# Kernel tuning notes

Measured on AMD Instinct MI355X. Metric: run time of the kernel, lower is better.

Reference implementation:

```python
import jax, jax.numpy as jnp
import numpy as np

E = 576        # embed_dims
HEADS = 18
NPTS = 12
NF = 3         # num_frames
DD = 2 * NF - 1  # depth of value volume (5)
HD = E // HEADS  # head dim (32)


def _grid_init_bias():
    # Faithful reproduction of init_weights() for sampling_offsets.bias
    theta = np.arange(8) * (2.0 * np.pi / 8)
    yaw = np.stack([np.cos(theta), np.sin(theta), np.zeros(8)], -1)
    roll = np.stack([np.zeros(8), np.cos(theta), np.sin(theta)], -1)
    pitch = np.stack([np.cos(theta), np.zeros(8), np.sin(theta)], -1)
    g = np.concatenate([yaw, pitch[[1, 2, 3, 5, 6, 7]], roll[[1, 3, 5, 7]]], 0)  # (18,3)
    g = g / np.abs(g).max(-1, keepdims=True)
    g = np.tile(g[:, None, None, :], (1, 1, NPTS, 1))              # (18,1,12,3)
    g = g * np.arange(1, NPTS + 1, dtype=np.float64)[None, None, :, None]
    return g.reshape(-1).astype(np.float32)                        # (18*12*3,)


def setup_inputs() -> dict:
    key = jax.random.key(0)
    ks = jax.random.split(key, 6)
    bs, h, w = 2, 64, 80
    nq = h * w
    lim = float(np.sqrt(6.0 / (E + E)))  # xavier uniform for square E x E
    return {
        "query": jax.random.normal(ks[0], (bs, nq, E), jnp.float32),
        "value": jax.random.normal(ks[1], (bs, nq * DD, E), jnp.float32),
        "query_pos": jax.random.normal(ks[2], (bs, nq, E), jnp.float32),
        "W_off": jnp.zeros((E, HEADS * NPTS * 3), jnp.float32),  # constant_init 0
        "b_off": jnp.asarray(_grid_init_bias()),
        "W_attn": jnp.zeros((E, HEADS * NPTS), jnp.float32),
        "b_attn": jnp.zeros((HEADS * NPTS,), jnp.float32),
        "W_v": jax.random.uniform(ks[3], (E, E), jnp.float32, -lim, lim),
        "b_v": jnp.zeros((E,), jnp.float32),
        "W_out": jax.random.uniform(ks[4], (E, E), jnp.float32, -lim, lim),
        "b_out": jnp.zeros((E,), jnp.float32),
        "h": 64,
        "w": 80,
    }


def _deform_attn_3d(value, loc, attn, D, H, W):
    # value: (bs, D*H*W, heads, hd)  token order: depth-major (D, H, W)
    # loc:   (bs, nq, heads, np, 3)  normalized (x, y, z) in [0,1]
    # attn:  (bs, nq, heads, np)
    bs, _, heads, hd = value.shape
    nq = loc.shape[1]
    # (bs, heads, D*H*W, hd) flat spatial for gathers
    v = value.reshape(bs, D, H, W, heads, hd).transpose(0, 4, 1, 2, 3, 5)
    v = v.reshape(bs, heads, D * H * W, hd)
    lt = jnp.moveaxis(loc, 2, 1)    # (bs, heads, nq, np, 3)
    at = jnp.moveaxis(attn, 2, 1)   # (bs, heads, nq, np)
    # grid_sample(align_corners=False) coordinate convention: pix = u*size - 0.5
    x = lt[..., 0] * W - 0.5
    y = lt[..., 1] * H - 0.5
    z = lt[..., 2] * D - 0.5
    x0 = jnp.floor(x); y0 = jnp.floor(y); z0 = jnp.floor(z)
    fx = x - x0; fy = y - y0; fz = z - z0
    acc = jnp.zeros((bs, heads, nq, NPTS, hd), v.dtype)
    for dz in (0, 1):
        for dy in (0, 1):
            for dx in (0, 1):
                xi = x0 + dx; yi = y0 + dy; zi = z0 + dz
                wgt = ((fx if dx else 1.0 - fx)
                       * (fy if dy else 1.0 - fy)
                       * (fz if dz else 1.0 - fz))
                valid = ((xi >= 0) & (xi < W) & (yi >= 0) & (yi < H)
                         & (zi >= 0) & (zi < D))
                xc = jnp.clip(xi, 0, W - 1).astype(jnp.int32)
                yc = jnp.clip(yi, 0, H - 1).astype(jnp.int32)
                zc = jnp.clip(zi, 0, D - 1).astype(jnp.int32)
                idx = ((zc * H + yc) * W + xc).reshape(bs, heads, nq * NPTS)
                g = jnp.take_along_axis(v, idx[..., None], axis=2)
                g = g.reshape(bs, heads, nq, NPTS, hd)
                acc = acc + g * (wgt * valid.astype(v.dtype))[..., None]
    out = jnp.einsum("bhqp,bhqpd->bhqd", at, acc)  # softmax-weighted sum over points
    return out.transpose(0, 2, 1, 3).reshape(bs, nq, heads * hd)


def _forward(query, value, query_pos, W_off, b_off, W_attn, b_attn,
             W_v, b_v, W_out, b_out, h, w):
    bs, nq, _ = query.shape
    q = query + query_pos
    v = (value @ W_v + b_v).reshape(bs, nq * DD, HEADS, HD)
    offs = (q @ W_off + b_off).reshape(bs, nq, HEADS, NPTS, 3)
    attn = jax.nn.softmax((q @ W_attn + b_attn).reshape(bs, nq, HEADS, NPTS), axis=-1)
    # reference points: pixel centers normalized, z = 0
    ry, rx = jnp.meshgrid((jnp.arange(h, dtype=jnp.float32) + 0.5) / h,
                          (jnp.arange(w, dtype=jnp.float32) + 0.5) / w,
                          indexing="ij")
    ref = jnp.stack([rx.reshape(-1), ry.reshape(-1),
                     jnp.zeros(h * w, jnp.float32)], -1)  # (nq, 3)
    norm = jnp.array([w, h, NF], jnp.float32)  # NOTE: z normalized by num_frames (as in source)
    loc = ref[None, :, None, None, :] + offs / norm
    out = _deform_attn_3d(v, loc, attn, DD, h, w)
    return out @ W_out + b_out  # dropout is identity at eval


def reference(query, value, query_pos, W_off, b_off, W_attn, b_attn,
              W_v, b_v, W_out, b_out, h, w):
    return _forward(query, value, query_pos, W_off, b_off, W_attn, b_attn,
                    W_v, b_v, W_out, b_out, h, w)
```

## Files before the change

kernel.cpp:

```cpp
#include <hip/hip_runtime.h>
#include <cstdint>

#define E_DIM   576
#define HEADS   18
#define NPTS    12
#define DDEPTH  5
#define HDIM    32
#define BSZ     2
#define GH      64
#define GW      80
#define NQ      (GH*GW)
#define NTOK    (NQ*DDEPTH)
#define MIXW    864
#define BQ_TOT  (BSZ*NQ)

typedef __attribute__((ext_vector_type(8))) short short8;
typedef __attribute__((ext_vector_type(4))) float f32x4;

__device__ __forceinline__ float b2f_lo(uint32_t u) {
    union { uint32_t u; float f; } v; v.u = u << 16; return v.f;
}
__device__ __forceinline__ float b2f_hi(uint32_t u) {
    union { uint32_t u; float f; } v; v.u = u & 0xffff0000u; return v.f;
}
__device__ __forceinline__ ushort f2b(float f) {
    union { float f; uint32_t u; } v; v.f = f;
    return (ushort)((v.u + 0x7fffu + ((v.u >> 16) & 1u)) >> 16);
}

__global__ void prep_all(const float* __restrict__ value,
                         const float* __restrict__ query, const float* __restrict__ query_pos,
                         const float* __restrict__ W_v, const float* __restrict__ W_out,
                         const float* __restrict__ W_off, const float* __restrict__ W_attn,
                         const float* __restrict__ b_off, const float* __restrict__ b_attn,
                         ushort* __restrict__ val_bf16, ushort* __restrict__ q_bf16,
                         ushort* __restrict__ wt_v, ushort* __restrict__ wt_out,
                         ushort* __restrict__ wt_mix, float* __restrict__ bias_mix) {
    const int i = blockIdx.x * blockDim.x + threadIdx.x;
    if (i < 51200 * 576 / 4) {
        const float4 v = reinterpret_cast<const float4*>(value)[i];
        ushort4 o; o.x = f2b(v.x); o.y = f2b(v.y); o.z = f2b(v.z); o.w = f2b(v.w);
        reinterpret_cast<ushort4*>(val_bf16)[i] = o;
    }
    if (i < 10240 * 576 / 4) {
        const float4 va = reinterpret_cast<const float4*>(query)[i];
        const float4 vb = reinterpret_cast<const float4*>(query_pos)[i];
        ushort4 o;
        o.x = f2b(va.x + vb.x); o.y = f2b(va.y + vb.y);
        o.z = f2b(va.z + vb.z); o.w = f2b(va.w + vb.w);
        reinterpret_cast<ushort4*>(q_bf16)[i] = o;
    }
    if (i < 864) bias_mix[i] = (i < 648) ? b_off[i] : b_attn[i - 648];
    if (i < 331776) {
        int n = i / E_DIM, k = i - n * E_DIM;
        wt_v[i] = f2b(W_v[(size_t)k * E_DIM + n]);
    } else if (i < 663552) {
        int j = i - 331776;
        int n = j / E_DIM, k = j - n * E_DIM;
        wt_out[j] = f2b(W_out[(size_t)k * E_DIM + n]);
    } else if (i < 1161216) {
        int j = i - 663552;
        int n = j / E_DIM, k = j - n * E_DIM;
        float v = (n < 648) ? W_off[(size_t)k * 648 + n] : W_attn[(size_t)k * 216 + (n - 648)];
        wt_mix[j] = f2b(v);
    }
}

#define TM 128
#define TN 96
#define BK 32

__device__ __forceinline__ void async_cp16(const ushort* gsrc, ushort* ldst) {
    __builtin_amdgcn_global_load_lds(
        (const __attribute__((address_space(1))) void*)gsrc,
        (__attribute__((address_space(3))) void*)ldst, 16, 0, 0);
}

__device__ __forceinline__ void xcd_map(int id, int total, int nbn, int& bx, int& by) {
    const int xcd = id & 7;
    const int pos = id >> 3;
    const int logical = xcd * (total >> 3) + pos;
    by = logical % nbn;
    bx = logical / nbn;
}

template <typename OutT>
__device__ __forceinline__ void gemm_body(ushort* __restrict__ smem, int bx, int by,
                                          const ushort* __restrict__ A,
                                          const ushort* __restrict__ Bt,
                                          const float* __restrict__ bias,
                                          OutT* __restrict__ C, int K, int ldc) {
    ushort* Asb = smem;
    ushort* Bsb = smem + TM * BK;
    const int tid  = threadIdx.x;
    const int wave = tid >> 6;
    const int lane = tid & 63;
    const int m16  = lane & 15;
    const int quad = lane >> 4;
    const int wr   = wave >> 1;
    const int wc   = wave & 1;
    const int row0 = bx * TM;
    const int n0   = by * TN;

    const f32x4 zero = {0.f, 0.f, 0.f, 0.f};
    f32x4 acc[4][3];
    #pragma unroll
    for (int rt = 0; rt < 4; ++rt)
        #pragma unroll
        for (int ct = 0; ct < 3; ++ct) acc[rt][ct] = zero;

    const int srow = lane >> 2;
    const int scol = (((lane & 3) ^ ((lane >> 3) & 3))) * 8;
    const int ksw  = (quad ^ ((m16 >> 1) & 3)) * 8;

    for (int k0 = 0; k0 < K; k0 += BK) {
        #pragma unroll
        for (int c = 0; c < 2; ++c) {
            const int ch = wave + c * 4;
            async_cp16(A + (size_t)(row0 + ch * 16 + srow) * K + k0 + scol,
                       Asb + ch * 512 + lane * 8);
        }
        async_cp16(Bt + (size_t)(n0 + wave * 16 + srow) * K + k0 + scol,
                   Bsb + wave * 512 + lane * 8);
        if (wave < 2)
            async_cp16(Bt + (size_t)(n0 + (wave + 4) * 16 + srow) * K + k0 + scol,
                       Bsb + (wave + 4) * 512 + lane * 8);
        __syncthreads();

        short8 afrag[4], bfrag[3];
        #pragma unroll
        for (int rt = 0; rt < 4; ++rt)
            afrag[rt] = *reinterpret_cast<const short8*>(
                Asb + (wr * 4 + rt) * 512 + m16 * 32 + ksw);
        #pragma unroll
        for (int ct = 0; ct < 3; ++ct)
            bfrag[ct] = *reinterpret_cast<const short8*>(
                Bsb + (wc * 3 + ct) * 512 + m16 * 32 + ksw);

        #pragma unroll
        for (int rt = 0; rt < 4; ++rt)
            #pragma unroll
            for (int ct = 0; ct < 3; ++ct)
                acc[rt][ct] = __builtin_amdgcn_mfma_f32_16x16x32_bf16(
                    afrag[rt], bfrag[ct], acc[rt][ct], 0, 0, 0);

        __syncthreads();
    }

    #pragma unroll
    for (int ct = 0; ct < 3; ++ct) {
        const int col = n0 + wc * 48 + ct * 16 + m16;
        const float bcol = bias[col];
        #pragma unroll
        for (int rt = 0; rt < 4; ++rt) {
            #pragma unroll
            for (int r = 0; r < 4; ++r) {
                const int row = row0 + wr * 64 + rt * 16 + quad * 4 + r;
                const float val = acc[rt][ct][r] + bcol;
                if constexpr (__is_same(OutT, float)) {
                    C[(size_t)row * ldc + col] = val;
                } else {
                    C[(size_t)row * ldc + col] = f2b(val);
                }
            }
        }
    }
}

template <typename OutT>
__global__ void gemm_mfma(const ushort* __restrict__ A, const ushort* __restrict__ Bt,
                          const float* __restrict__ bias, OutT* __restrict__ C,
                          int K, int ldc, int total, int nbn) {
    __shared__ __align__(16) ushort smem[(TM + TN) * BK];
    int bx, by;
    xcd_map(blockIdx.x, total, nbn, bx, by);
    gemm_body<OutT>(smem, bx, by, A, Bt, bias, C, K, ldc);
}

__global__ void gemm_dual(const ushort* __restrict__ A1, const ushort* __restrict__ B1,
                          const float* __restrict__ bias1, float* __restrict__ C1,
                          int K1, int ldc1, int nbn1, int split,
                          const ushort* __restrict__ A2, const ushort* __restrict__ B2,
                          const float* __restrict__ bias2, ushort* __restrict__ C2,
                          int K2, int ldc2, int nbn2, int total2) {
    __shared__ __align__(16) ushort smem[(TM + TN) * BK];
    const int id = blockIdx.x;
    int bx, by;
    if (id < split) {
        xcd_map(id, split, nbn1, bx, by);
        gemm_body<float>(smem, bx, by, A1, B1, bias1, C1, K1, ldc1);
    } else {
        xcd_map(id - split, total2, nbn2, bx, by);
        gemm_body<ushort>(smem, bx, by, A2, B2, bias2, C2, K2, ldc2);
    }
}

__global__ void __launch_bounds__(256, 8)
deform_kernel(const ushort* __restrict__ vbuf,
              const float* __restrict__ mix,
              ushort* __restrict__ aout) {
    __shared__ uint2 corn[16 * 97];
    __shared__ int   ccnt[16];
    const int gl   = threadIdx.x >> 4;
    const int l    = threadIdx.x & 15;
    const int head = blockIdx.x / 640;
    const int bq   = (blockIdx.x % 640) * 16 + gl;
    const int q    = bq % NQ;
    const int b    = bq / NQ;
    const int qx   = q % GW;
    const int qy   = q / GW;

    const float* mrow = mix + (size_t)bq * MIXW;

    float lg = (l < NPTS) ? mrow[648 + head * NPTS + l] : -1e30f;
    float mx = lg;
    #pragma unroll
    for (int mk = 1; mk < 16; mk <<= 1) mx = fmaxf(mx, __shfl_xor(mx, mk, 16));
    float e = (l < NPTS) ? __expf(lg - mx) : 0.f;
    float s = e;
    #pragma unroll
    for (int mk = 1; mk < 16; mk <<= 1) s += __shfl_xor(s, mk, 16);

    float    cw[8];
    uint32_t coff[8];
    uint32_t mask = 0;
    {
        const float ap = e / s;
        const int pl = (l < NPTS) ? l : 0;
        const int ob = (head * NPTS + pl) * 3;
        const float ox = mrow[ob + 0];
        const float oy = mrow[ob + 1];
        const float oz = mrow[ob + 2];
        const float x = (float)qx + ox;
        const float y = (float)qy + oy;
        const float z = oz * (5.0f / 3.0f) - 0.5f;
        const float x0f = floorf(x), y0f = floorf(y), z0f = floorf(z);
        const int x0 = (int)x0f, y0 = (int)y0f, z0 = (int)z0f;
        const float fx = x - x0f, fy = y - y0f, fz = z - z0f;

        #pragma unroll
        for (int dz = 0; dz < 2; ++dz) {
            const int zi = z0 + dz;
            const bool zv = (zi >= 0) & (zi < DDEPTH);
            const int zc = min(max(zi, 0), DDEPTH - 1);
            const float wz = dz ? fz : 1.f - fz;
            #pragma unroll
            for (int dy = 0; dy < 2; ++dy) {
                const int yi = y0 + dy;
                const bool yv = (yi >= 0) & (yi < GH);
                const int yc = min(max(yi, 0), GH - 1);
                const float wy = dy ? fy : 1.f - fy;
                #pragma unroll
                for (int dx = 0; dx < 2; ++dx) {
                    const int xi = x0 + dx;
                    const bool xv = (xi >= 0) & (xi < GW);
                    const int xc = min(max(xi, 0), GW - 1);
                    const float wx = dx ? fx : 1.f - fx;
                    const int i = dz * 4 + dy * 2 + dx;
                    const bool valid = zv & yv & xv & (l < NPTS);
                    cw[i]   = ap * wz * wy * wx;
                    coff[i] = (uint32_t)((zc * GH + yc) * GW + xc) * (E_DIM / 2);
                    mask |= (valid ? (1u << i) : 0u);
                }
            }
        }
    }

    const int cnt = __popc(mask);
    int pre = cnt;
    #pragma unroll
    for (int mk = 1; mk < 16; mk <<= 1) {
        const int t = __shfl_up(pre, mk, 16);
        if (l >= mk) pre += t;
    }
    int o = gl * 97 + (pre - cnt);
    #pragma unroll
    for (int i = 0; i < 8; ++i) {
        if (mask & (1u << i)) {
            uint2 w; w.x = __float_as_uint(cw[i]); w.y = coff[i];
            corn[o] = w;
            ++o;
        }
    }
    if (l == 15) ccnt[gl] = pre;
    __syncthreads();

    const uint32_t lbase = (uint32_t)b * (uint32_t)(NTOK * (E_DIM / 2))
                         + (uint32_t)(head * (HDIM / 2) + l);
    const uint32_t* vb32 = reinterpret_cast<const uint32_t*>(vbuf);
    const int n = ccnt[gl];
    const uint2* cg = &corn[gl * 97];
    float o0 = 0.f, o1 = 0.f;
    #pragma unroll 2
    for (int j = 0; j < n; ++j) {
        const uint2 wo = cg[j];
        const uint32_t pair = vb32[lbase + wo.y];
        const float w = __uint_as_float(wo.x);
        o0 += w * b2f_lo(pair);
        o1 += w * b2f_hi(pair);
    }
    const uint32_t packed = (uint32_t)f2b(o0) | ((uint32_t)f2b(o1) << 16);
    reinterpret_cast<uint32_t*>(aout)[(size_t)bq * (E_DIM / 2) + head * (HDIM / 2) + l] = packed;
}

extern "C" void kernel_launch(void* const* d_in, const int* in_sizes, int n_in,
                              void* d_out, int out_size, void* d_ws, size_t ws_size,
                              hipStream_t stream) {
    const float* query     = (const float*)d_in[0];
    const float* value     = (const float*)d_in[1];
    const float* query_pos = (const float*)d_in[2];
    const float* W_off     = (const float*)d_in[3];
    const float* b_off     = (const float*)d_in[4];
    const float* W_attn    = (const float*)d_in[5];
    const float* b_attn    = (const float*)d_in[6];
    const float* W_v       = (const float*)d_in[7];
    const float* b_v       = (const float*)d_in[8];
    const float* W_out     = (const float*)d_in[9];
    const float* b_out     = (const float*)d_in[10];
    float* out = (float*)d_out;

    char* ws = (char*)d_ws;
    ushort* vbuf     = (ushort*)(ws);
    ushort* val_bf16 = (ushort*)(ws + 58982400);
    ushort* aout     = val_bf16;
    ushort* q_bf16   = (ushort*)(ws + 117964800);
    float*  mixb     = (float*) (ws + 129761280);
    ushort* wt_v     = (ushort*)(ws + 165150720);
    ushort* wt_out   = (ushort*)(ws + 165814272);
    ushort* wt_mix   = (ushort*)(ws + 166477824);
    float*  bias_mix = (float*) (ws + 167473152);

    prep_all<<<(51200 * 576 / 4) / 256, 256, 0, stream>>>(
        value, query, query_pos, W_v, W_out, W_off, W_attn, b_off, b_attn,
        val_bf16, q_bf16, wt_v, wt_out, wt_mix, bias_mix);

    gemm_dual<<<720 + 2400, 256, 0, stream>>>(
        q_bf16, wt_mix, bias_mix, mixb, E_DIM, MIXW, 9, 720,
        val_bf16, wt_v, b_v, vbuf, E_DIM, E_DIM, 6, 2400);

    deform_kernel<<<HEADS * 640, 256, 0, stream>>>(vbuf, mixb, aout);

    gemm_mfma<float><<<480, 256, 0, stream>>>(
        aout, wt_out, b_out, out, E_DIM, E_DIM, 480, 6);
}
```

Before: 357.5 us.

## Fuse fp32-to-bf16 input conversion and query+pos add into GEMM A-tile loads

Removes the separate prep pass that converted value and query+query_pos to bf16 in global memory. The dual GEMM now loads fp32 A rows directly, adds query_pos for the mix GEMM, converts to bf16 in registers, and writes swizzled tiles into LDS. This avoids a full round-trip of the large value tensor (write and re-read in bf16). The cost is that A loads become synchronous register loads instead of async global-to-LDS copies, and the GEMM reads twice as many bytes for A.

```diff
diff --git a/kernel.cpp b/kernel.cpp
--- a/kernel.cpp
+++ b/kernel.cpp
@@ -16,6 +16,7 @@
 
 typedef __attribute__((ext_vector_type(8))) short short8;
 typedef __attribute__((ext_vector_type(4))) float f32x4;
+typedef __attribute__((ext_vector_type(4))) uint32_t u32x4;
 
 __device__ __forceinline__ float b2f_lo(uint32_t u) {
     union { uint32_t u; float f; } v; v.u = u << 16; return v.f;
@@ -28,38 +29,22 @@
     return (ushort)((v.u + 0x7fffu + ((v.u >> 16) & 1u)) >> 16);
 }
 
-__global__ void prep_all(const float* __restrict__ value,
-                         const float* __restrict__ query, const float* __restrict__ query_pos,
-                         const float* __restrict__ W_v, const float* __restrict__ W_out,
-                         const float* __restrict__ W_off, const float* __restrict__ W_attn,
-                         const float* __restrict__ b_off, const float* __restrict__ b_attn,
-                         ushort* __restrict__ val_bf16, ushort* __restrict__ q_bf16,
-                         ushort* __restrict__ wt_v, ushort* __restrict__ wt_out,
-                         ushort* __restrict__ wt_mix, float* __restrict__ bias_mix) {
-    const int i = blockIdx.x * blockDim.x + threadIdx.x;
-    if (i < 51200 * 576 / 4) {
-        const float4 v = reinterpret_cast<const float4*>(value)[i];
-        ushort4 o; o.x = f2b(v.x); o.y = f2b(v.y); o.z = f2b(v.z); o.w = f2b(v.w);
-        reinterpret_cast<ushort4*>(val_bf16)[i] = o;
-    }
-    if (i < 10240 * 576 / 4) {
-        const float4 va = reinterpret_cast<const float4*>(query)[i];
-        const float4 vb = reinterpret_cast<const float4*>(query_pos)[i];
-        ushort4 o;
-        o.x = f2b(va.x + vb.x); o.y = f2b(va.y + vb.y);
-        o.z = f2b(va.z + vb.z); o.w = f2b(va.w + vb.w);
-        reinterpret_cast<ushort4*>(q_bf16)[i] = o;
-    }
-    if (i < 864) bias_mix[i] = (i < 648) ? b_off[i] : b_attn[i - 648];
-    if (i < 331776) {
-        int n = i / E_DIM, k = i - n * E_DIM;
-        wt_v[i] = f2b(W_v[(size_t)k * E_DIM + n]);
-    } else if (i < 663552) {
-        int j = i - 331776;
+__global__ void prep_weights(const float* __restrict__ W_v, const float* __restrict__ W_out,
+                             const float* __restrict__ W_off, const float* __restrict__ W_attn,
+                             const float* __restrict__ b_off, const float* __restrict__ b_attn,
+                             ushort* __restrict__ wt_v, ushort* __restrict__ wt_out,
+                             ushort* __restrict__ wt_mix, float* __restrict__ bias_mix) {
+    int idx = blockIdx.x * blockDim.x + threadIdx.x;
+    if (idx < 864) bias_mix[idx] = (idx < 648) ? b_off[idx] : b_attn[idx - 648];
+    if (idx < 331776) {
+        int n = idx / E_DIM, k = idx - n * E_DIM;
+        wt_v[idx] = f2b(W_v[(size_t)k * E_DIM + n]);
+    } else if (idx < 663552) {
+        int j = idx - 331776;
         int n = j / E_DIM, k = j - n * E_DIM;
         wt_out[j] = f2b(W_out[(size_t)k * E_DIM + n]);
-    } else if (i < 1161216) {
-        int j = i - 663552;
+    } else if (idx < 1161216) {
+        int j = idx - 663552;
         int n = j / E_DIM, k = j - n * E_DIM;
         float v = (n < 648) ? W_off[(size_t)k * 648 + n] : W_attn[(size_t)k * 216 + (n - 648)];
         wt_mix[j] = f2b(v);
@@ -69,6 +54,10 @@
 #define TM 128
 #define TN 96
 #define BK 32
+
+#define AM_BF16   0
+#define AM_F32    1
+#define AM_F32ADD 2
 
 __device__ __forceinline__ void async_cp16(const ushort* gsrc, ushort* ldst) {
     __builtin_amdgcn_global_load_lds(
@@ -84,9 +73,10 @@
     bx = logical / nbn;
 }
 
-template <typename OutT>
+template <int AMODE, typename OutT>
 __device__ __forceinline__ void gemm_body(ushort* __restrict__ smem, int bx, int by,
-                                          const ushort* __restrict__ A,
+                                          const void* __restrict__ Apv,
+                                          const float* __restrict__ A2,
                                           const ushort* __restrict__ Bt,
                                           const float* __restrict__ bias,
                                           OutT* __restrict__ C, int K, int ldc) {
@@ -113,18 +103,63 @@
     const int scol = (((lane & 3) ^ ((lane >> 3) & 3))) * 8;
     const int ksw  = (quad ^ ((m16 >> 1) & 3)) * 8;
 
+    const int srow_f = ((wave & 1) << 6) | lane;
+    const int khalf  = wave >> 1;
+    const float* A32  = (const float*)Apv;
+    const ushort* A16 = (const ushort*)Apv;
+    const float* arow  = A32 + (size_t)(row0 + srow_f) * K + khalf * 16;
+    const float* arow2 = (AMODE == AM_F32ADD)
+                         ? A2 + (size_t)(row0 + srow_f) * K + khalf * 16 : nullptr;
+
     for (int k0 = 0; k0 < K; k0 += BK) {
-        #pragma unroll
-        for (int c = 0; c < 2; ++c) {
-            const int ch = wave + c * 4;
-            async_cp16(A + (size_t)(row0 + ch * 16 + srow) * K + k0 + scol,
-                       Asb + ch * 512 + lane * 8);
+        float4 av0, av1, av2, av3, bv0, bv1, bv2, bv3;
+        if constexpr (AMODE == AM_BF16) {
+            #pragma unroll
+            for (int c = 0; c < 2; ++c) {
+                const int ch = wave + c * 4;
+                async_cp16(A16 + (size_t)(row0 + ch * 16 + srow) * K + k0 + scol,
+                           Asb + ch * 512 + lane * 8);
+            }
+        } else {
+            av0 = *reinterpret_cast<const float4*>(arow + k0);
+            av1 = *reinterpret_cast<const float4*>(arow + k0 + 4);
+            av2 = *reinterpret_cast<const float4*>(arow + k0 + 8);
+            av3 = *reinterpret_cast<const float4*>(arow + k0 + 12);
+            if constexpr (AMODE == AM_F32ADD) {
+                bv0 = *reinterpret_cast<const float4*>(arow2 + k0);
+                bv1 = *reinterpret_cast<const float4*>(arow2 + k0 + 4);
+                bv2 = *reinterpret_cast<const float4*>(arow2 + k0 + 8);
+                bv3 = *reinterpret_cast<const float4*>(arow2 + k0 + 12);
+            }
         }
         async_cp16(Bt + (size_t)(n0 + wave * 16 + srow) * K + k0 + scol,
                    Bsb + wave * 512 + lane * 8);
         if (wave < 2)
             async_cp16(Bt + (size_t)(n0 + (wave + 4) * 16 + srow) * K + k0 + scol,
                        Bsb + (wave + 4) * 512 + lane * 8);
+
+        if constexpr (AMODE != AM_BF16) {
+            if constexpr (AMODE == AM_F32ADD) {
+                av0.x += bv0.x; av0.y += bv0.y; av0.z += bv0.z; av0.w += bv0.w;
+                av1.x += bv1.x; av1.y += bv1.y; av1.z += bv1.z; av1.w += bv1.w;
+                av2.x += bv2.x; av2.y += bv2.y; av2.z += bv2.z; av2.w += bv2.w;
+                av3.x += bv3.x; av3.y += bv3.y; av3.z += bv3.z; av3.w += bv3.w;
+            }
+            const int r  = srow_f & 15;
+            const int ck = srow_f >> 4;
+            const int xr = (r >> 1) & 3;
+            const int s0 = khalf * 2;
+            u32x4 w0 = {(uint32_t)f2b(av0.x) | ((uint32_t)f2b(av0.y) << 16),
+                        (uint32_t)f2b(av0.z) | ((uint32_t)f2b(av0.w) << 16),
+                        (uint32_t)f2b(av1.x) | ((uint32_t)f2b(av1.y) << 16),
+                        (uint32_t)f2b(av1.z) | ((uint32_t)f2b(av1.w) << 16)};
+            u32x4 w1 = {(uint32_t)f2b(av2.x) | ((uint32_t)f2b(av2.y) << 16),
+                        (uint32_t)f2b(av2.z) | ((uint32_t)f2b(av2.w) << 16),
+                        (uint32_t)f2b(av3.x) | ((uint32_t)f2b(av3.y) << 16),
+                        (uint32_t)f2b(av3.z) | ((uint32_t)f2b(av3.w) << 16)};
+            *reinterpret_cast<u32x4*>(&Asb[ck * 512 + r * 32 + ((s0 ^ xr) * 8)]) = w0;
+            *reinterpret_cast<u32x4*>(&Asb[ck * 512 + r * 32 + (((s0 + 1) ^ xr) * 8)]) = w1;
+        }
         __syncthreads();
 
         short8 afrag[4], bfrag[3];
@@ -167,20 +202,20 @@
     }
 }
 
-template <typename OutT>
-__global__ void gemm_mfma(const ushort* __restrict__ A, const ushort* __restrict__ Bt,
-                          const float* __restrict__ bias, OutT* __restrict__ C,
-                          int K, int ldc, int total, int nbn) {
+__global__ void gemm_out(const ushort* __restrict__ A, const ushort* __restrict__ Bt,
+                         const float* __restrict__ bias, float* __restrict__ C,
+                         int K, int ldc, int total, int nbn) {
     __shared__ __align__(16) ushort smem[(TM + TN) * BK];
     int bx, by;
     xcd_map(blockIdx.x, total, nbn, bx, by);
-    gemm_body<OutT>(smem, bx, by, A, Bt, bias, C, K, ldc);
-}
-
-__global__ void gemm_dual(const ushort* __restrict__ A1, const ushort* __restrict__ B1,
+    gemm_body<AM_BF16, float>(smem, bx, by, A, nullptr, Bt, bias, C, K, ldc);
+}
+
+__global__ void gemm_dual(const float* __restrict__ q, const float* __restrict__ qp,
+                          const ushort* __restrict__ B1,
                           const float* __restrict__ bias1, float* __restrict__ C1,
                           int K1, int ldc1, int nbn1, int split,
-                          const ushort* __restrict__ A2, const ushort* __restrict__ B2,
+                          const float* __restrict__ val, const ushort* __restrict__ B2,
                           const float* __restrict__ bias2, ushort* __restrict__ C2,
                           int K2, int ldc2, int nbn2, int total2) {
     __shared__ __align__(16) ushort smem[(TM + TN) * BK];
@@ -188,10 +223,10 @@
     int bx, by;
     if (id < split) {
         xcd_map(id, split, nbn1, bx, by);
-        gemm_body<float>(smem, bx, by, A1, B1, bias1, C1, K1, ldc1);
+        gemm_body<AM_F32ADD, float>(smem, bx, by, q, qp, B1, bias1, C1, K1, ldc1);
     } else {
         xcd_map(id - split, total2, nbn2, bx, by);
-        gemm_body<ushort>(smem, bx, by, A2, B2, bias2, C2, K2, ldc2);
+        gemm_body<AM_F32, ushort>(smem, bx, by, val, nullptr, B2, bias2, C2, K2, ldc2);
     }
 }
 
@@ -321,25 +356,22 @@
 
     char* ws = (char*)d_ws;
     ushort* vbuf     = (ushort*)(ws);
-    ushort* val_bf16 = (ushort*)(ws + 58982400);
-    ushort* aout     = val_bf16;
-    ushort* q_bf16   = (ushort*)(ws + 117964800);
-    float*  mixb     = (float*) (ws + 129761280);
-    ushort* wt_v     = (ushort*)(ws + 165150720);
-    ushort* wt_out   = (ushort*)(ws + 165814272);
-    ushort* wt_mix   = (ushort*)(ws + 166477824);
-    float*  bias_mix = (float*) (ws + 167473152);
-
-    prep_all<<<(51200 * 576 / 4) / 256, 256, 0, stream>>>(
-        value, query, query_pos, W_v, W_out, W_off, W_attn, b_off, b_attn,
-        val_bf16, q_bf16, wt_v, wt_out, wt_mix, bias_mix);
+    ushort* aout     = (ushort*)(ws + 58982400);
+    float*  mixb     = (float*) (ws + 70778880);
+    ushort* wt_v     = (ushort*)(ws + 106168320);
+    ushort* wt_out   = (ushort*)(ws + 106831872);
+    ushort* wt_mix   = (ushort*)(ws + 107495424);
+    float*  bias_mix = (float*) (ws + 108490752);
+
+    prep_weights<<<(1161216 + 255) / 256, 256, 0, stream>>>(
+        W_v, W_out, W_off, W_attn, b_off, b_attn, wt_v, wt_out, wt_mix, bias_mix);
 
     gemm_dual<<<720 + 2400, 256, 0, stream>>>(
-        q_bf16, wt_mix, bias_mix, mixb, E_DIM, MIXW, 9, 720,
-        val_bf16, wt_v, b_v, vbuf, E_DIM, E_DIM, 6, 2400);
+        query, query_pos, wt_mix, bias_mix, mixb, E_DIM, MIXW, 9, 720,
+        value, wt_v, b_v, vbuf, E_DIM, E_DIM, 6, 2400);
 
     deform_kernel<<<HEADS * 640, 256, 0, stream>>>(vbuf, mixb, aout);
 
-    gemm_mfma<float><<<480, 256, 0, stream>>>(
+    gemm_out<<<480, 256, 0, stream>>>(
         aout, wt_out, b_out, out, E_DIM, E_DIM, 480, 6);
 }
```

Measured after the change: 433.5 us. 21.3% more time.
